# Optimization experiments

Hardware: AMD Instinct MI355X
Metric: run time of the kernel (lower is better)

Reference implementation:

```python
import jax, jax.numpy as jnp
import numpy as np

B, N, E, H = 4, 4096, 1024, 16
D = E // H            # head_dim = 64
P_DIM = 64            # proj_dim; feature dim = 2*P_DIM = 128
EPS = 1e-4


def setup_inputs() -> dict:
    key = jax.random.key(0)
    ks = jax.random.split(key, 9)
    x = jax.random.normal(ks[0], (B, N, E), jnp.float32)
    init = 0.02
    Wq = jax.random.normal(ks[1], (E, E), jnp.float32) * init
    Wk = jax.random.normal(ks[2], (E, E), jnp.float32) * init
    Wv = jax.random.normal(ks[3], (E, E), jnp.float32) * init
    Wo = jax.random.normal(ks[4], (E, E), jnp.float32) * init
    bq = jnp.zeros((E,), jnp.float32)
    bk = jnp.zeros((E,), jnp.float32)
    bv = jnp.zeros((E,), jnp.float32)
    bo = jnp.zeros((E,), jnp.float32)
    # orthogonal random projection matrix (proj_dim, head_dim), fixed (non-trainable)
    g = np.random.default_rng(0).normal(size=(P_DIM, D))
    P = jnp.asarray(np.linalg.qr(g)[0], jnp.float32)
    return dict(x=x, Wq=Wq, bq=bq, Wk=Wk, bk=bk, Wv=Wv, bv=bv, Wo=Wo, bo=bo, P=P)


def _heads(z):
    # (B, N, E) -> (B, H, N, D)
    return z.reshape(B, N, H, D).transpose(0, 2, 1, 3)


def _normalize(z):
    return z / (jnp.linalg.norm(z, axis=-1, keepdims=True) + EPS)


def reference(x, Wq, bq, Wk, bk, Wv, bv, Wo, bo, P):
    q = _heads(x @ Wq.T + bq)
    k = _heads(x @ Wk.T + bk)
    v = _heads(x @ Wv.T + bv)
    q = _normalize(q)
    k = _normalize(k)
    scale = H ** 0.25
    qp = jnp.einsum('bhnd,ed->bhne', q, P) * scale
    kp = jnp.einsum('bhnd,ed->bhne', k, P) * scale
    fscale = P_DIM ** (-0.5)   # x.shape[-1]**-0.5 with last dim = proj_dim
    qf = jnp.concatenate([jnp.sin(qp), jnp.cos(qp)], axis=-1) * fscale  # (B,H,N,2p)
    kf = jnp.concatenate([jnp.sin(kp), jnp.cos(kp)], axis=-1) * fscale
    # non-causal linear attention: q @ (k^T v)
    kv = jnp.einsum('bhme,bhmd->bhed', kf, v)          # (B,H,2p,D)
    o = jnp.einsum('bhne,bhed->bhnd', qf, kv)          # (B,H,N,D)
    o = o.transpose(0, 2, 1, 3).reshape(B, N, E)
    return o @ Wo.T + bo
```

## Files before the change

kernel.cpp:

```cpp
#include <hip/hip_runtime.h>
#include <hip/hip_bf16.h>
#include <stdint.h>


typedef __bf16 bf16x8 __attribute__((ext_vector_type(8)));
typedef float f32x4 __attribute__((ext_vector_type(4)));

#define AS1 __attribute__((address_space(1)))
#define AS3 __attribute__((address_space(3)))

__device__ __forceinline__ void gl2lds16(const void* g, void* l) {
    __builtin_amdgcn_global_load_lds((const AS1 void*)g, (AS3 void*)l, 16, 0, 0);
}

#define CFENCE asm volatile("" ::: "memory")

static constexpr int GM = 16384, GN = 1024, GK = 1024;
static constexpr int KV_SLABS = 8;

__global__ void detect_kernel(const unsigned short* __restrict__ x,
                              int* __restrict__ flag) {
    __shared__ int s;
    const int lane = threadIdx.x;
    if (lane == 0) s = 0;
    __syncthreads();
    int cnt = 0;
#pragma unroll
    for (int i = 0; i < 2; ++i) {
        const unsigned short u = x[i * 64 + lane];
        const int e = (u >> 7) & 0xFF;
        cnt += (e >= 117 && e <= 131) ? 1 : 0;
    }
    atomicAdd(&s, cnt);
    __syncthreads();
    if (lane == 0) *flag = (s >= 100) ? 1 : 0;
}

__device__ __forceinline__ void cvt8(const float* s, __hip_bfloat16* d) {
    const float4 a = *(const float4*)s;
    const float4 b = *(const float4*)(s + 4);
    union { uint4 u; __hip_bfloat16 h[8]; } pk;
    pk.h[0] = __float2bfloat16(a.x); pk.h[1] = __float2bfloat16(a.y);
    pk.h[2] = __float2bfloat16(a.z); pk.h[3] = __float2bfloat16(a.w);
    pk.h[4] = __float2bfloat16(b.x); pk.h[5] = __float2bfloat16(b.y);
    pk.h[6] = __float2bfloat16(b.z); pk.h[7] = __float2bfloat16(b.w);
    *(uint4*)d = pk.u;
}

__global__ __launch_bounds__(256) void cvt_kernel(
    const void* __restrict__ src, __hip_bfloat16* __restrict__ dst,
    int n, const int* __restrict__ flag) {
    if (*flag) return;
    const int i = (blockIdx.x * 256 + threadIdx.x) * 8;
    if (i >= n) return;
    cvt8((const float*)src + i, dst + i);
}

__global__ __launch_bounds__(256) void cvt4_kernel(
    const void* __restrict__ s0, __hip_bfloat16* __restrict__ d0,
    const void* __restrict__ s1, __hip_bfloat16* __restrict__ d1,
    const void* __restrict__ s2, __hip_bfloat16* __restrict__ d2,
    const void* __restrict__ s3, __hip_bfloat16* __restrict__ d3,
    const int* __restrict__ flag) {
    if (*flag) return;
    const int which = blockIdx.x >> 9;
    const int i = ((blockIdx.x & 511) * 256 + threadIdx.x) * 8;
    const float* s = (const float*)(which == 0 ? s0 : which == 1 ? s1
                                   : which == 2 ? s2 : s3) + i;
    __hip_bfloat16* d = (which == 0 ? d0 : which == 1 ? d1
                         : which == 2 ? d2 : d3) + i;
    cvt8(s, d);
}

__global__ __launch_bounds__(256, 2) void gemm2_kernel(
    const void* __restrict__ Adirect,
    const __hip_bfloat16* __restrict__ Acvt,
    const void* __restrict__ W0r, const __hip_bfloat16* __restrict__ W0c,
    const void* __restrict__ W1r, const __hip_bfloat16* __restrict__ W1c,
    const void* __restrict__ b0r, const void* __restrict__ b1r,
    void* __restrict__ o0, void* __restrict__ o1,
    const int* __restrict__ flag)
{
    __shared__ unsigned short smem[3 * 128 * 64];
    unsigned short* sA  = smem;
    unsigned short* sB0 = smem + 128 * 64;
    unsigned short* sB1 = smem + 2 * 128 * 64;

    const int tid  = threadIdx.x;
    const int lane = tid & 63;
    const int w    = tid >> 6;
    const int wm   = w >> 1, wn = w & 1;
    const int lr   = lane & 15, lk = lane >> 4;

    const int id    = blockIdx.x;
    const int xcd   = id & 7;
    const int slot  = id >> 3;
    const int m0    = (xcd * 16 + (slot & 15)) * 128;
    const int n0    = (slot >> 4) * 128;
    const int fl    = *flag;

    const __hip_bfloat16* A  = fl ? (const __hip_bfloat16*)Adirect : Acvt;
    const __hip_bfloat16* W0 = fl ? (const __hip_bfloat16*)W0r : W0c;
    const __hip_bfloat16* W1 = fl ? (const __hip_bfloat16*)W1r : W1c;

    f32x4 acc[2][4][4];
#pragma unroll
    for (int t = 0; t < 2; ++t)
#pragma unroll
        for (int i = 0; i < 4; ++i)
#pragma unroll
            for (int j = 0; j < 4; ++j)
                acc[t][i][j] = (f32x4){0.f, 0.f, 0.f, 0.f};

    const __hip_bfloat16* Ab  = A + (size_t)m0 * GK;
    const __hip_bfloat16* W0b = W0 + (size_t)n0 * GK;
    const __hip_bfloat16* W1b = W1 + (size_t)n0 * GK;

    for (int k0 = 0; k0 < GK; k0 += 64) {
#pragma unroll
        for (int j = 0; j < 4; ++j) {
            const int chunk = j * 256 + tid;
            const int row   = chunk >> 3;
            const int c     = chunk & 7;
            const int cs    = c ^ (row & 7);
            const size_t go = (size_t)row * GK + k0 + cs * 8;
            const int lo = (j * 256 + w * 64) * 16;
            gl2lds16(Ab  + go, (char*)sA  + lo);
            gl2lds16(W0b + go, (char*)sB0 + lo);
            gl2lds16(W1b + go, (char*)sB1 + lo);
        }
        __syncthreads();
#pragma unroll
        for (int kk = 0; kk < 64; kk += 32) {
            const int jj = ((kk >> 3) + lk) ^ (lr & 7);
            bf16x8 af[4], b0f[4], b1f[4];
#pragma unroll
            for (int i = 0; i < 4; ++i)
                af[i] = *(const bf16x8*)&sA[(wm * 64 + i * 16 + lr) * 64 + jj * 8];
#pragma unroll
            for (int j = 0; j < 4; ++j)
                b0f[j] = *(const bf16x8*)&sB0[(wn * 64 + j * 16 + lr) * 64 + jj * 8];
#pragma unroll
            for (int j = 0; j < 4; ++j)
                b1f[j] = *(const bf16x8*)&sB1[(wn * 64 + j * 16 + lr) * 64 + jj * 8];
#pragma unroll
            for (int i = 0; i < 4; ++i)
#pragma unroll
                for (int j = 0; j < 4; ++j) {
                    acc[0][i][j] = __builtin_amdgcn_mfma_f32_16x16x32_bf16(
                        af[i], b0f[j], acc[0][i][j], 0, 0, 0);
                    acc[1][i][j] = __builtin_amdgcn_mfma_f32_16x16x32_bf16(
                        af[i], b1f[j], acc[1][i][j], 0, 0, 0);
                }
        }
        __syncthreads();
    }

    __hip_bfloat16* sC = (__hip_bfloat16*)smem;
#pragma unroll
    for (int t = 0; t < 2; ++t) {
        const void* bias_raw = t ? b1r : b0r;
        void* Cout = t ? o1 : o0;
#pragma unroll
        for (int j = 0; j < 4; ++j) {
            const int col = wn * 64 + j * 16 + lr;
            const float bv = fl ? __bfloat162float(((const __hip_bfloat16*)bias_raw)[n0 + col])
                                : ((const float*)bias_raw)[n0 + col];
            const int c2 = col >> 3, o = col & 7;
#pragma unroll
            for (int i = 0; i < 4; ++i) {
                const int rb = wm * 64 + i * 16 + lk * 4;
#pragma unroll
                for (int r = 0; r < 4; ++r) {
                    const int row = rb + r;
                    sC[row * 128 + (c2 ^ (row & 7)) * 8 + o] =
                        __float2bfloat16(acc[t][i][j][r] + bv);
                }
            }
        }
        __syncthreads();
        {
            const int row = tid >> 1, hf = tid & 1;
            __hip_bfloat16* dst = (__hip_bfloat16*)Cout + (size_t)(m0 + row) * GN + n0 + hf * 64;
#pragma unroll
            for (int q = 0; q < 8; ++q) {
                const int cc = (hf * 8 + q) ^ (row & 7);
                *(uint4*)(dst + q * 8) = *(const uint4*)&sC[row * 128 + cc * 8];
            }
        }
        __syncthreads();
    }
}

__global__ __launch_bounds__(512, 2) void gemm256_kernel(
    const void* __restrict__ Adirect,
    const __hip_bfloat16* __restrict__ Acvt,
    const void* __restrict__ Wr, const __hip_bfloat16* __restrict__ Wc,
    const void* __restrict__ bias_raw,
    void* __restrict__ Cout,
    const int* __restrict__ flag, int last)
{
    __shared__ unsigned short smem[65536];

    const int tid  = threadIdx.x;
    const int lane = tid & 63;
    const int w    = tid >> 6;
    const int wm   = w >> 2, wn = w & 3;
    const int lr   = lane & 15, lk = lane >> 4;

    const int id  = blockIdx.x;
    const int xcd = id & 7;
    const int s   = id >> 3;
    const int m0  = (xcd * 8 + (s >> 2)) * 256;
    const int n0  = (s & 3) * 256;
    const int fl  = *flag;

    const __hip_bfloat16* A = fl ? (const __hip_bfloat16*)Adirect : Acvt;
    const __hip_bfloat16* W = fl ? (const __hip_bfloat16*)Wr : Wc;
    const __hip_bfloat16* Ab = A + (size_t)m0 * GK;
    const __hip_bfloat16* Wb = W + (size_t)n0 * GK;

    f32x4 acc[8][4];
#pragma unroll
    for (int i = 0; i < 8; ++i)
#pragma unroll
        for (int j = 0; j < 4; ++j)
            acc[i][j] = (f32x4){0.f, 0.f, 0.f, 0.f};

    const int jj8 = (lk ^ ((lr >> 1) & 3)) * 8;
    int offA[8], offB[4];
#pragma unroll
    for (int i = 0; i < 8; ++i)
        offA[i] = (wm * 128 + i * 16 + lr) * 32 + jj8;
#pragma unroll
    for (int j = 0; j < 4; ++j)
        offB[j] = 8192 + (wn * 64 + j * 16 + lr) * 32 + jj8;

    size_t gofs[2];
    int    ldso[2];
#pragma unroll
    for (int p = 0; p < 2; ++p) {
        const int chunk = p * 512 + tid;
        const int row   = chunk >> 2, c = chunk & 3;
        const int cs    = c ^ ((row >> 1) & 3);
        gofs[p] = (size_t)row * GK + cs * 8;
        ldso[p] = (p * 512 + w * 64) * 16;
    }

    auto stage2 = [&](int t, int part) {
        char* base = (char*)smem + (t & 3) * 32768 + ldso[part];
        const size_t go = gofs[part] + (size_t)(t * 32);
        gl2lds16(Ab + go, base);
        gl2lds16(Wb + go, base + 16384);
    };

    stage2(0, 0); stage2(0, 1);
    stage2(1, 0); stage2(1, 1);
    stage2(2, 0); stage2(2, 1);
    asm volatile("s_waitcnt vmcnt(8)" ::: "memory");
    __builtin_amdgcn_s_barrier();

    auto tile = [&](int slot, int t, bool do_stage, int gate) {
        const unsigned short* sl = smem + slot * 16384;
        bf16x8 af[4], bfr[4], af2[4];
#pragma unroll
        for (int i = 0; i < 4; ++i) af[i] = *(const bf16x8*)&sl[offA[i]];
#pragma unroll
        for (int j = 0; j < 4; ++j) bfr[j] = *(const bf16x8*)&sl[offB[j]];
        if (do_stage) stage2(t + 3, 0);
        CFENCE;
        __builtin_amdgcn_s_barrier();
        __builtin_amdgcn_s_setprio(1);
#pragma unroll
        for (int i = 0; i < 4; ++i)
#pragma unroll
            for (int j = 0; j < 4; ++j)
                acc[i][j] = __builtin_amdgcn_mfma_f32_16x16x32_bf16(
                    af[i], bfr[j], acc[i][j], 0, 0, 0);
        __builtin_amdgcn_s_setprio(0);
        CFENCE;
        __builtin_amdgcn_s_barrier();
#pragma unroll
        for (int i = 0; i < 4; ++i) af2[i] = *(const bf16x8*)&sl[offA[4 + i]];
        if (do_stage) stage2(t + 3, 1);
        if (gate == 8)      asm volatile("s_waitcnt vmcnt(8)" ::: "memory");
        else if (gate == 4) asm volatile("s_waitcnt vmcnt(4)" ::: "memory");
        else                asm volatile("s_waitcnt vmcnt(0)" ::: "memory");
        __builtin_amdgcn_s_barrier();
        __builtin_amdgcn_s_setprio(1);
#pragma unroll
        for (int i = 0; i < 4; ++i)
#pragma unroll
            for (int j = 0; j < 4; ++j)
                acc[4 + i][j] = __builtin_amdgcn_mfma_f32_16x16x32_bf16(
                    af2[i], bfr[j], acc[4 + i][j], 0, 0, 0);
        __builtin_amdgcn_s_setprio(0);
        CFENCE;
        __builtin_amdgcn_s_barrier();
    };

#pragma unroll 1
    for (int t = 0; t < 28; t += 4) {
        tile(0, t + 0, true, 8);
        tile(1, t + 1, true, 8);
        tile(2, t + 2, true, 8);
        tile(3, t + 3, true, 8);
    }
    tile(0, 28, true, 8);
    tile(1, 29, false, 4);
    tile(2, 30, false, 0);
    tile(3, 31, false, 0);

    const bool f32out = (last != 0) && (fl == 0);
    if (f32out) {
#pragma unroll
        for (int j = 0; j < 4; ++j) {
            const int col = n0 + wn * 64 + j * 16 + lr;
            const float bv = ((const float*)bias_raw)[col];
#pragma unroll
            for (int i = 0; i < 8; ++i) {
                const int rbase = m0 + wm * 128 + i * 16 + lk * 4;
#pragma unroll
                for (int r = 0; r < 4; ++r)
                    ((float*)Cout)[(size_t)(rbase + r) * GN + col] =
                        acc[i][j][r] + bv;
            }
        }
        return;
    }

    unsigned short* sC = smem;
#pragma unroll
    for (int j = 0; j < 4; ++j) {
        const int col = wn * 64 + j * 16 + lr;
        const float bv = fl ? __bfloat162float(((const __hip_bfloat16*)bias_raw)[n0 + col])
                            : ((const float*)bias_raw)[n0 + col];
        const int c_hi = col >> 3, off = col & 7;
#pragma unroll
        for (int i = 0; i < 8; ++i) {
            const int rb = wm * 128 + i * 16 + lk * 4;
#pragma unroll
            for (int r = 0; r < 4; ++r) {
                const int row = rb + r;
                const int phys = c_hi ^ (row & 7);
                __hip_bfloat16 hv = __float2bfloat16(acc[i][j][r] + bv);
                sC[row * 256 + phys * 8 + off] = *(unsigned short*)&hv;
            }
        }
    }
    __syncthreads();
    {
        const int row = tid >> 1, half = tid & 1;
        __hip_bfloat16* dst = (__hip_bfloat16*)Cout +
            (size_t)(m0 + row) * GN + n0 + half * 128;
#pragma unroll
        for (int q = 0; q < 16; ++q) {
            const int chunk = half * 16 + q;
            const int phys  = chunk ^ (row & 7);
            *(uint4*)(dst + q * 8) = *(const uint4*)&sC[row * 256 + phys * 8];
        }
    }
}

__device__ __forceinline__ void load_P(const void* Praw, int f,
                                       __hip_bfloat16* sP, int tid) {
    const int e = tid >> 2, q = tid & 3;
    union { uint4 u[2]; __hip_bfloat16 h[16]; } pk;
    if (f) {
        pk.u[0] = *(const uint4*)((const __hip_bfloat16*)Praw + e * 64 + q * 16);
        pk.u[1] = *(const uint4*)((const __hip_bfloat16*)Praw + e * 64 + q * 16 + 8);
    } else {
        const float* ps = (const float*)Praw + e * 64 + q * 16;
#pragma unroll
        for (int j = 0; j < 16; ++j) pk.h[j] = __float2bfloat16(ps[j]);
    }
    *(uint4*)&sP[e * 72 + q * 16]     = pk.u[0];
    *(uint4*)&sP[e * 72 + q * 16 + 8] = pk.u[1];
}

__device__ __forceinline__ float sumsq16(uint4 a, uint4 b) {
    union { uint4 u; __hip_bfloat16 h[8]; } x0, x1;
    x0.u = a; x1.u = b;
    float ss = 0.f;
#pragma unroll
    for (int j = 0; j < 8; ++j) {
        float v0 = __bfloat162float(x0.h[j]); ss += v0 * v0;
        float v1 = __bfloat162float(x1.h[j]); ss += v1 * v1;
    }
    return ss;
}

__global__ __launch_bounds__(256) void kv_kernel(
    const __hip_bfloat16* __restrict__ Km,
    const __hip_bfloat16* __restrict__ Vm,
    const void* __restrict__ Praw,
    float* __restrict__ PKV,
    const int* __restrict__ flag)
{
    __shared__ __hip_bfloat16 sK[64 * 72];
    __shared__ __hip_bfloat16 sVT[64 * 72];
    __shared__ __hip_bfloat16 sP[64 * 72];
    __shared__ __hip_bfloat16 sKFT[128 * 72];
    __shared__ float sRN[64];

    const int tid  = threadIdx.x;
    const int lane = tid & 63;
    const int w    = tid >> 6;
    const int lr   = lane & 15, lk = lane >> 4;
    const int bh   = blockIdx.y;
    const int b    = bh >> 4, h = bh & 15;
    const int nst  = blockIdx.x * 512;
    const int f    = *flag;
    const int n    = tid >> 2, q2 = tid & 3;

    load_P(Praw, f, sP, tid);

    f32x4 acck[2][4];
#pragma unroll
    for (int i = 0; i < 2; ++i)
#pragma unroll
        for (int j = 0; j < 4; ++j)
            acck[i][j] = (f32x4){0.f, 0.f, 0.f, 0.f};

    size_t base = ((size_t)(b * 4096 + nst + n)) * 1024 + h * 64 + q2 * 16;
    uint4 ka = *(const uint4*)(Km + base), kb = *(const uint4*)(Km + base + 8);
    uint4 va = *(const uint4*)(Vm + base), vb = *(const uint4*)(Vm + base + 8);

    for (int s = 0; s < 8; ++s) {
        __syncthreads();
        *(uint4*)&sK[n * 72 + q2 * 16]     = ka;
        *(uint4*)&sK[n * 72 + q2 * 16 + 8] = kb;
        {
            union { uint4 u[2]; __hip_bfloat16 h[16]; } vv;
            vv.u[0] = va; vv.u[1] = vb;
#pragma unroll
            for (int j = 0; j < 16; ++j) sVT[(q2 * 16 + j) * 72 + n] = vv.h[j];
        }
        {
            float ss = sumsq16(ka, kb);
            ss += __shfl_xor(ss, 1, 64);
            ss += __shfl_xor(ss, 2, 64);
            if (q2 == 0) sRN[n] = 2.0f / (sqrtf(ss) + 1e-4f);
        }
        if (s < 7) {
            base = ((size_t)(b * 4096 + nst + (s + 1) * 64 + n)) * 1024 + h * 64 + q2 * 16;
            ka = *(const uint4*)(Km + base); kb = *(const uint4*)(Km + base + 8);
            va = *(const uint4*)(Vm + base); vb = *(const uint4*)(Vm + base + 8);
        }
        {
            bf16x8 afr0 = *(const bf16x8*)&sK[(w * 16 + lr) * 72 + lk * 8];
            bf16x8 afr1 = *(const bf16x8*)&sK[(w * 16 + lr) * 72 + 32 + lk * 8];
            float rn[4];
#pragma unroll
            for (int r = 0; r < 4; ++r) rn[r] = sRN[w * 16 + lk * 4 + r];
#pragma unroll
            for (int eb = 0; eb < 4; ++eb) {
                f32x4 pa = (f32x4){0.f, 0.f, 0.f, 0.f};
                bf16x8 b0 = *(const bf16x8*)&sP[(eb * 16 + lr) * 72 + lk * 8];
                bf16x8 b1 = *(const bf16x8*)&sP[(eb * 16 + lr) * 72 + 32 + lk * 8];
                pa = __builtin_amdgcn_mfma_f32_16x16x32_bf16(afr0, b0, pa, 0, 0, 0);
                pa = __builtin_amdgcn_mfma_f32_16x16x32_bf16(afr1, b1, pa, 0, 0, 0);
                const int col = eb * 16 + lr;
#pragma unroll
                for (int r = 0; r < 4; ++r) {
                    const int row = w * 16 + lk * 4 + r;
                    float sv, cv;
                    __sincosf(pa[r] * rn[r], &sv, &cv);
                    sKFT[col * 72 + row]        = __float2bfloat16(sv * 0.125f);
                    sKFT[(col + 64) * 72 + row] = __float2bfloat16(cv * 0.125f);
                }
            }
        }
        __syncthreads();
#pragma unroll
        for (int ks = 0; ks < 2; ++ks) {
            bf16x8 a2[2], b2[4];
            a2[0] = *(const bf16x8*)&sKFT[(w * 16 + lr) * 72 + ks * 32 + lk * 8];
            a2[1] = *(const bf16x8*)&sKFT[((w + 4) * 16 + lr) * 72 + ks * 32 + lk * 8];
#pragma unroll
            for (int db = 0; db < 4; ++db)
                b2[db] = *(const bf16x8*)&sVT[(db * 16 + lr) * 72 + ks * 32 + lk * 8];
#pragma unroll
            for (int i = 0; i < 2; ++i)
#pragma unroll
                for (int db = 0; db < 4; ++db)
                    acck[i][db] = __builtin_amdgcn_mfma_f32_16x16x32_bf16(
                        a2[i], b2[db], acck[i][db], 0, 0, 0);
        }
    }

    float* out = PKV + ((size_t)blockIdx.x * 64 + bh) * 8192;
#pragma unroll
    for (int i = 0; i < 2; ++i)
#pragma unroll
        for (int db = 0; db < 4; ++db)
#pragma unroll
            for (int r = 0; r < 4; ++r) {
                const int e = (w + 4 * i) * 16 + lk * 4 + r;
                const int d = db * 16 + lr;
                out[e * 64 + d] = acck[i][db][r];
            }
}

__global__ __launch_bounds__(256) void kv_reduce_kernel(
    const float* __restrict__ PKV, float* __restrict__ gKV)
{
    const int i = (blockIdx.x * 256 + threadIdx.x) * 4;
    f32x4 s = (f32x4){0.f, 0.f, 0.f, 0.f};
#pragma unroll
    for (int sl = 0; sl < KV_SLABS; ++sl) {
        const float4 v = *(const float4*)(PKV + (size_t)sl * 64 * 8192 + i);
        s[0] += v.x; s[1] += v.y; s[2] += v.z; s[3] += v.w;
    }
    *(float4*)(gKV + i) = *(float4*)&s;
}

__global__ __launch_bounds__(256) void o_kernel(
    const __hip_bfloat16* __restrict__ Qm,
    const void* __restrict__ Praw,
    const float* __restrict__ gKV,
    __hip_bfloat16* __restrict__ O,
    const int* __restrict__ flag)
{
    __shared__ __hip_bfloat16 sQ[64 * 72];
    __shared__ __hip_bfloat16 sP[64 * 72];
    __shared__ __hip_bfloat16 sQF[64 * 136];
    __shared__ __hip_bfloat16 sKVT[64 * 136];
    __shared__ float sRN[64];

    const int tid  = threadIdx.x;
    const int lane = tid & 63;
    const int w    = tid >> 6;
    const int lr   = lane & 15, lk = lane >> 4;
    const int bh   = blockIdx.y;
    const int b    = bh >> 4, h = bh & 15;
    const int nst  = blockIdx.x * 256;
    const int f    = *flag;
    const int n    = tid >> 2, q2 = tid & 3;

    load_P(Praw, f, sP, tid);
    {
        const float* kvsrc = gKV + (size_t)bh * 8192;
        for (int t = tid; t < 8192; t += 256) {
            const int e = t >> 6, d = t & 63;
            sKVT[d * 136 + e] = __float2bfloat16(kvsrc[t]);
        }
    }

    size_t base = ((size_t)(b * 4096 + nst + n)) * 1024 + h * 64 + q2 * 16;
    uint4 qa = *(const uint4*)(Qm + base), qb = *(const uint4*)(Qm + base + 8);

    __syncthreads();

    for (int s = 0; s < 4; ++s) {
        const int gn0 = nst + s * 64;
        *(uint4*)&sQ[n * 72 + q2 * 16]     = qa;
        *(uint4*)&sQ[n * 72 + q2 * 16 + 8] = qb;
        {
            float ss = sumsq16(qa, qb);
            ss += __shfl_xor(ss, 1, 64);
            ss += __shfl_xor(ss, 2, 64);
            if (q2 == 0) sRN[n] = 2.0f / (sqrtf(ss) + 1e-4f);
        }
        if (s < 3) {
            base = ((size_t)(b * 4096 + nst + (s + 1) * 64 + n)) * 1024 + h * 64 + q2 * 16;
            qa = *(const uint4*)(Qm + base); qb = *(const uint4*)(Qm + base + 8);
        }
        {
            bf16x8 afr0 = *(const bf16x8*)&sQ[(w * 16 + lr) * 72 + lk * 8];
            bf16x8 afr1 = *(const bf16x8*)&sQ[(w * 16 + lr) * 72 + 32 + lk * 8];
            float rn[4];
#pragma unroll
            for (int r = 0; r < 4; ++r) rn[r] = sRN[w * 16 + lk * 4 + r];
#pragma unroll
            for (int eb = 0; eb < 4; ++eb) {
                f32x4 pa = (f32x4){0.f, 0.f, 0.f, 0.f};
                bf16x8 b0 = *(const bf16x8*)&sP[(eb * 16 + lr) * 72 + lk * 8];
                bf16x8 b1 = *(const bf16x8*)&sP[(eb * 16 + lr) * 72 + 32 + lk * 8];
                pa = __builtin_amdgcn_mfma_f32_16x16x32_bf16(afr0, b0, pa, 0, 0, 0);
                pa = __builtin_amdgcn_mfma_f32_16x16x32_bf16(afr1, b1, pa, 0, 0, 0);
                const int col = eb * 16 + lr;
#pragma unroll
                for (int r = 0; r < 4; ++r) {
                    const int row = w * 16 + lk * 4 + r;
                    float sv, cv;
                    __sincosf(pa[r] * rn[r], &sv, &cv);
                    sQF[row * 136 + col]      = __float2bfloat16(sv * 0.125f);
                    sQF[row * 136 + 64 + col] = __float2bfloat16(cv * 0.125f);
                }
            }
        }
        f32x4 oacc[4];
#pragma unroll
        for (int nb = 0; nb < 4; ++nb) oacc[nb] = (f32x4){0.f, 0.f, 0.f, 0.f};
#pragma unroll
        for (int ks = 0; ks < 4; ++ks) {
            bf16x8 aa = *(const bf16x8*)&sQF[(w * 16 + lr) * 136 + ks * 32 + lk * 8];
#pragma unroll
            for (int nb = 0; nb < 4; ++nb) {
                bf16x8 bb = *(const bf16x8*)&sKVT[(nb * 16 + lr) * 136 + ks * 32 + lk * 8];
                oacc[nb] = __builtin_amdgcn_mfma_f32_16x16x32_bf16(aa, bb, oacc[nb], 0, 0, 0);
            }
        }
#pragma unroll
        for (int nb = 0; nb < 4; ++nb)
#pragma unroll
            for (int r = 0; r < 4; ++r)
                sQ[(w * 16 + lk * 4 + r) * 72 + nb * 16 + lr] =
                    __float2bfloat16(oacc[nb][r]);
        {
            uint4 o0 = *(uint4*)&sQ[n * 72 + q2 * 16];
            uint4 o1 = *(uint4*)&sQ[n * 72 + q2 * 16 + 8];
            const size_t obase = ((size_t)(b * 4096 + gn0 + n)) * 1024 + h * 64 + q2 * 16;
            *(uint4*)(O + obase)     = o0;
            *(uint4*)(O + obase + 8) = o1;
        }
    }
}

extern "C" void kernel_launch(void* const* d_in, const int* in_sizes, int n_in,
                              void* d_out, int out_size, void* d_ws, size_t ws_size,
                              hipStream_t stream)
{
    (void)in_sizes; (void)n_in; (void)out_size; (void)ws_size;
    const void* x  = d_in[0];
    const void* Wq = d_in[1];
    const void* bq = d_in[2];
    const void* Wk = d_in[3];
    const void* bk = d_in[4];
    const void* Wv = d_in[5];
    const void* bv = d_in[6];
    const void* Wo = d_in[7];
    const void* bo = d_in[8];
    const void* P  = d_in[9];

    constexpr size_t XE = (size_t)GM * GN;
    constexpr size_t WE = (size_t)GN * GK;
    constexpr size_t KVE = (size_t)64 * 128 * 64;

    __hip_bfloat16* xb  = (__hip_bfloat16*)d_ws;
    __hip_bfloat16* wqb = xb + XE;
    __hip_bfloat16* wkb = wqb + WE;
    __hip_bfloat16* wvb = wkb + WE;
    __hip_bfloat16* wob = wvb + WE;
    __hip_bfloat16* R1  = wob + WE;
    __hip_bfloat16* R2  = R1 + XE;
    float* gKV = (float*)(R2 + XE);
    float* PKV = gKV + KVE;
    int* flag  = (int*)(PKV + (size_t)KV_SLABS * 64 * 8192);

    dim3 blk(256);
    hipLaunchKernelGGL(detect_kernel, dim3(1), dim3(64), 0, stream,
                       (const unsigned short*)x, flag);

    hipLaunchKernelGGL(cvt_kernel, dim3(8192), blk, 0, stream, x, xb, (int)XE, flag);
    hipLaunchKernelGGL(cvt4_kernel, dim3(2048), blk, 0, stream,
                       Wq, wqb, Wk, wkb, Wv, wvb, Wo, wob, flag);

    hipLaunchKernelGGL(gemm2_kernel, dim3(1024), blk, 0, stream,
                       x, xb, Wk, wkb, Wv, wvb, bk, bv, R1, R2, flag);
    hipLaunchKernelGGL(kv_kernel, dim3(KV_SLABS, 64), blk, 0, stream, R1, R2, P, PKV, flag);
    hipLaunchKernelGGL(kv_reduce_kernel, dim3(512), blk, 0, stream, PKV, gKV);
    hipLaunchKernelGGL(gemm256_kernel, dim3(256), dim3(512), 0, stream,
                       x, xb, Wq, wqb, bq, R2, flag, 0);
    hipLaunchKernelGGL(o_kernel, dim3(16, 64), blk, 0, stream, R2, P, gKV, R1, flag);
    hipLaunchKernelGGL(gemm256_kernel, dim3(256), dim3(512), 0, stream,
                       R1, R1, Wo, wob, bo, d_out, flag, 1);
}
```

Baseline: 364.4 us.

## Shrink single-GEMM tile to 128x256 with double buffering and split KV wider

Replaces the 256x256 four-stage GEMM used for the Q and output projections with a 128x256 tile, a two-slot LDS double buffer and a simpler per-k-step loop. This doubles the grid to 512 blocks so the GPU's compute units are better filled. It also halves per-block LDS use. The KV accumulation kernel now uses 16 slabs of 256 rows instead of 8 of 512, for more parallelism. The cost is less reuse of B tiles per block, shallower prefetch, and more partial KV slabs to reduce.

```diff
diff --git a/kernel.cpp b/kernel.cpp
--- a/kernel.cpp
+++ b/kernel.cpp
@@ -16,7 +16,7 @@
 #define CFENCE asm volatile("" ::: "memory")
 
 static constexpr int GM = 16384, GN = 1024, GK = 1024;
-static constexpr int KV_SLABS = 8;
+static constexpr int KV_SLABS = 16;
 
 __global__ void detect_kernel(const unsigned short* __restrict__ x,
                               int* __restrict__ flag) {
@@ -192,7 +192,7 @@
     }
 }
 
-__global__ __launch_bounds__(512, 2) void gemm256_kernel(
+__global__ __launch_bounds__(512, 2) void gemm1_kernel(
     const void* __restrict__ Adirect,
     const __hip_bfloat16* __restrict__ Acvt,
     const void* __restrict__ Wr, const __hip_bfloat16* __restrict__ Wc,
@@ -200,7 +200,7 @@
     void* __restrict__ Cout,
     const int* __restrict__ flag, int last)
 {
-    __shared__ unsigned short smem[65536];
+    __shared__ unsigned short smem[32768];
 
     const int tid  = threadIdx.x;
     const int lane = tid & 63;
@@ -211,8 +211,8 @@
     const int id  = blockIdx.x;
     const int xcd = id & 7;
     const int s   = id >> 3;
-    const int m0  = (xcd * 8 + (s >> 2)) * 256;
-    const int n0  = (s & 3) * 256;
+    const int m0  = (xcd * 16 + (s & 15)) * 128;
+    const int n0  = (s >> 4) * 256;
     const int fl  = *flag;
 
     const __hip_bfloat16* A = fl ? (const __hip_bfloat16*)Adirect : Acvt;
@@ -220,56 +220,47 @@
     const __hip_bfloat16* Ab = A + (size_t)m0 * GK;
     const __hip_bfloat16* Wb = W + (size_t)n0 * GK;
 
-    f32x4 acc[8][4];
-#pragma unroll
-    for (int i = 0; i < 8; ++i)
+    f32x4 acc[4][4];
+#pragma unroll
+    for (int i = 0; i < 4; ++i)
 #pragma unroll
         for (int j = 0; j < 4; ++j)
             acc[i][j] = (f32x4){0.f, 0.f, 0.f, 0.f};
 
     const int jj8 = (lk ^ ((lr >> 1) & 3)) * 8;
-    int offA[8], offB[4];
-#pragma unroll
-    for (int i = 0; i < 8; ++i)
-        offA[i] = (wm * 128 + i * 16 + lr) * 32 + jj8;
+    int offA[4], offB[4];
+#pragma unroll
+    for (int i = 0; i < 4; ++i)
+        offA[i] = (wm * 64 + i * 16 + lr) * 32 + jj8;
 #pragma unroll
     for (int j = 0; j < 4; ++j)
-        offB[j] = 8192 + (wn * 64 + j * 16 + lr) * 32 + jj8;
-
-    size_t gofs[2];
-    int    ldso[2];
+        offB[j] = 4096 + (wn * 64 + j * 16 + lr) * 32 + jj8;
+
+    const int rowA = tid >> 2, cA = tid & 3;
+    const size_t goA = (size_t)rowA * GK + (size_t)((cA ^ ((rowA >> 1) & 3)) * 8);
+    size_t goB[2];
 #pragma unroll
     for (int p = 0; p < 2; ++p) {
         const int chunk = p * 512 + tid;
         const int row   = chunk >> 2, c = chunk & 3;
-        const int cs    = c ^ ((row >> 1) & 3);
-        gofs[p] = (size_t)row * GK + cs * 8;
-        ldso[p] = (p * 512 + w * 64) * 16;
-    }
-
-    auto stage2 = [&](int t, int part) {
-        char* base = (char*)smem + (t & 3) * 32768 + ldso[part];
-        const size_t go = gofs[part] + (size_t)(t * 32);
-        gl2lds16(Ab + go, base);
-        gl2lds16(Wb + go, base + 16384);
+        goB[p] = (size_t)row * GK + (size_t)((c ^ ((row >> 1) & 3)) * 8);
+    }
+
+    auto stage = [&](int t, int slot) {
+        char* base = (char*)smem + slot * 24576;
+        const size_t k = (size_t)(t * 32);
+        gl2lds16(Ab + goA + k,    base + w * 1024);
+        gl2lds16(Wb + goB[0] + k, base + 8192 + w * 1024);
+        gl2lds16(Wb + goB[1] + k, base + 16384 + w * 1024);
     };
 
-    stage2(0, 0); stage2(0, 1);
-    stage2(1, 0); stage2(1, 1);
-    stage2(2, 0); stage2(2, 1);
-    asm volatile("s_waitcnt vmcnt(8)" ::: "memory");
-    __builtin_amdgcn_s_barrier();
-
-    auto tile = [&](int slot, int t, bool do_stage, int gate) {
-        const unsigned short* sl = smem + slot * 16384;
-        bf16x8 af[4], bfr[4], af2[4];
+    auto compute = [&](int slot) {
+        const unsigned short* sl = smem + slot * 12288;
+        bf16x8 af[4], bfr[4];
 #pragma unroll
         for (int i = 0; i < 4; ++i) af[i] = *(const bf16x8*)&sl[offA[i]];
 #pragma unroll
         for (int j = 0; j < 4; ++j) bfr[j] = *(const bf16x8*)&sl[offB[j]];
-        if (do_stage) stage2(t + 3, 0);
-        CFENCE;
-        __builtin_amdgcn_s_barrier();
         __builtin_amdgcn_s_setprio(1);
 #pragma unroll
         for (int i = 0; i < 4; ++i)
@@ -278,38 +269,28 @@
                 acc[i][j] = __builtin_amdgcn_mfma_f32_16x16x32_bf16(
                     af[i], bfr[j], acc[i][j], 0, 0, 0);
         __builtin_amdgcn_s_setprio(0);
+    };
+
+    stage(0, 0); stage(1, 1);
+    asm volatile("s_waitcnt vmcnt(3)" ::: "memory");
+    __builtin_amdgcn_s_barrier();
+
+    constexpr int NT = GK / 32;
+#pragma unroll 1
+    for (int t = 0; t < NT - 1; ++t) {
+        compute(t & 1);
         CFENCE;
         __builtin_amdgcn_s_barrier();
-#pragma unroll
-        for (int i = 0; i < 4; ++i) af2[i] = *(const bf16x8*)&sl[offA[4 + i]];
-        if (do_stage) stage2(t + 3, 1);
-        if (gate == 8)      asm volatile("s_waitcnt vmcnt(8)" ::: "memory");
-        else if (gate == 4) asm volatile("s_waitcnt vmcnt(4)" ::: "memory");
-        else                asm volatile("s_waitcnt vmcnt(0)" ::: "memory");
+        if (t < NT - 2) {
+            stage(t + 2, t & 1);
+            asm volatile("s_waitcnt vmcnt(3)" ::: "memory");
+        } else {
+            asm volatile("s_waitcnt vmcnt(0)" ::: "memory");
+        }
         __builtin_amdgcn_s_barrier();
-        __builtin_amdgcn_s_setprio(1);
-#pragma unroll
-        for (int i = 0; i < 4; ++i)
-#pragma unroll
-            for (int j = 0; j < 4; ++j)
-                acc[4 + i][j] = __builtin_amdgcn_mfma_f32_16x16x32_bf16(
-                    af2[i], bfr[j], acc[4 + i][j], 0, 0, 0);
-        __builtin_amdgcn_s_setprio(0);
-        CFENCE;
-        __builtin_amdgcn_s_barrier();
-    };
-
-#pragma unroll 1
-    for (int t = 0; t < 28; t += 4) {
-        tile(0, t + 0, true, 8);
-        tile(1, t + 1, true, 8);
-        tile(2, t + 2, true, 8);
-        tile(3, t + 3, true, 8);
-    }
-    tile(0, 28, true, 8);
-    tile(1, 29, false, 4);
-    tile(2, 30, false, 0);
-    tile(3, 31, false, 0);
+    }
+    compute((NT - 1) & 1);
+    __syncthreads();
 
     const bool f32out = (last != 0) && (fl == 0);
     if (f32out) {
@@ -318,8 +299,8 @@
             const int col = n0 + wn * 64 + j * 16 + lr;
             const float bv = ((const float*)bias_raw)[col];
 #pragma unroll
-            for (int i = 0; i < 8; ++i) {
-                const int rbase = m0 + wm * 128 + i * 16 + lk * 4;
+            for (int i = 0; i < 4; ++i) {
+                const int rbase = m0 + wm * 64 + i * 16 + lk * 4;
 #pragma unroll
                 for (int r = 0; r < 4; ++r)
                     ((float*)Cout)[(size_t)(rbase + r) * GN + col] =
@@ -337,8 +318,8 @@
                             : ((const float*)bias_raw)[n0 + col];
         const int c_hi = col >> 3, off = col & 7;
 #pragma unroll
-        for (int i = 0; i < 8; ++i) {
-            const int rb = wm * 128 + i * 16 + lk * 4;
+        for (int i = 0; i < 4; ++i) {
+            const int rb = wm * 64 + i * 16 + lk * 4;
 #pragma unroll
             for (int r = 0; r < 4; ++r) {
                 const int row = rb + r;
@@ -350,14 +331,14 @@
     }
     __syncthreads();
     {
-        const int row = tid >> 1, half = tid & 1;
+        const int row = tid >> 2, q = tid & 3;
         __hip_bfloat16* dst = (__hip_bfloat16*)Cout +
-            (size_t)(m0 + row) * GN + n0 + half * 128;
-#pragma unroll
-        for (int q = 0; q < 16; ++q) {
-            const int chunk = half * 16 + q;
+            (size_t)(m0 + row) * GN + n0 + q * 64;
+#pragma unroll
+        for (int qq = 0; qq < 8; ++qq) {
+            const int chunk = q * 8 + qq;
             const int phys  = chunk ^ (row & 7);
-            *(uint4*)(dst + q * 8) = *(const uint4*)&sC[row * 256 + phys * 8];
+            *(uint4*)(dst + qq * 8) = *(const uint4*)&sC[row * 256 + phys * 8];
         }
     }
 }
@@ -409,7 +390,7 @@
     const int lr   = lane & 15, lk = lane >> 4;
     const int bh   = blockIdx.y;
     const int b    = bh >> 4, h = bh & 15;
-    const int nst  = blockIdx.x * 512;
+    const int nst  = blockIdx.x * 256;
     const int f    = *flag;
     const int n    = tid >> 2, q2 = tid & 3;
 
@@ -426,7 +407,7 @@
     uint4 ka = *(const uint4*)(Km + base), kb = *(const uint4*)(Km + base + 8);
     uint4 va = *(const uint4*)(Vm + base), vb = *(const uint4*)(Vm + base + 8);
 
-    for (int s = 0; s < 8; ++s) {
+    for (int s = 0; s < 4; ++s) {
         __syncthreads();
         *(uint4*)&sK[n * 72 + q2 * 16]     = ka;
         *(uint4*)&sK[n * 72 + q2 * 16 + 8] = kb;
@@ -442,7 +423,7 @@
             ss += __shfl_xor(ss, 2, 64);
             if (q2 == 0) sRN[n] = 2.0f / (sqrtf(ss) + 1e-4f);
         }
-        if (s < 7) {
+        if (s < 3) {
             base = ((size_t)(b * 4096 + nst + (s + 1) * 64 + n)) * 1024 + h * 64 + q2 * 16;
             ka = *(const uint4*)(Km + base); kb = *(const uint4*)(Km + base + 8);
             va = *(const uint4*)(Vm + base); vb = *(const uint4*)(Vm + base + 8);
@@ -661,9 +642,9 @@
                        x, xb, Wk, wkb, Wv, wvb, bk, bv, R1, R2, flag);
     hipLaunchKernelGGL(kv_kernel, dim3(KV_SLABS, 64), blk, 0, stream, R1, R2, P, PKV, flag);
     hipLaunchKernelGGL(kv_reduce_kernel, dim3(512), blk, 0, stream, PKV, gKV);
-    hipLaunchKernelGGL(gemm256_kernel, dim3(256), dim3(512), 0, stream,
+    hipLaunchKernelGGL(gemm1_kernel, dim3(512), dim3(512), 0, stream,
                        x, xb, Wq, wqb, bq, R2, flag, 0);
     hipLaunchKernelGGL(o_kernel, dim3(16, 64), blk, 0, stream, R2, P, gKV, R1, flag);
-    hipLaunchKernelGGL(gemm256_kernel, dim3(256), dim3(512), 0, stream,
+    hipLaunchKernelGGL(gemm1_kernel, dim3(512), dim3(512), 0, stream,
                        R1, R1, Wo, wob, bo, d_out, flag, 1);
 }
```

After: 391.9 us. 7.5% more time.

## Double-buffer K=32 LDS stages in fused QK GEMM with prefetch overlap

Applied to the files above, without the earlier changes.

Restructures the dual-output GEMM main loop from single-buffered K=64 tiles with two barriers per iteration to double-buffered K=32 stages. The next stage's global-to-LDS loads are issued before computing the current one, with one barrier per step, so memory latency can overlap MFMA work. It also precomputes load and fragment offsets with a new XOR swizzle, and raises wave priority around the MFMA block. LDS use stays the same, but there are twice as many loop iterations and barriers, and each barrier still waits on vmcnt(0), which limits how much overlap is possible.

```diff
diff --git a/kernel.cpp b/kernel.cpp
--- a/kernel.cpp
+++ b/kernel.cpp
@@ -81,10 +81,7 @@
     void* __restrict__ o0, void* __restrict__ o1,
     const int* __restrict__ flag)
 {
-    __shared__ unsigned short smem[3 * 128 * 64];
-    unsigned short* sA  = smem;
-    unsigned short* sB0 = smem + 128 * 64;
-    unsigned short* sB1 = smem + 2 * 128 * 64;
+    __shared__ unsigned short smem[24576];
 
     const int tid  = threadIdx.x;
     const int lane = tid & 63;
@@ -116,45 +113,72 @@
     const __hip_bfloat16* W0b = W0 + (size_t)n0 * GK;
     const __hip_bfloat16* W1b = W1 + (size_t)n0 * GK;
 
-    for (int k0 = 0; k0 < GK; k0 += 64) {
-#pragma unroll
-        for (int j = 0; j < 4; ++j) {
-            const int chunk = j * 256 + tid;
-            const int row   = chunk >> 3;
-            const int c     = chunk & 7;
-            const int cs    = c ^ (row & 7);
-            const size_t go = (size_t)row * GK + k0 + cs * 8;
-            const int lo = (j * 256 + w * 64) * 16;
-            gl2lds16(Ab  + go, (char*)sA  + lo);
-            gl2lds16(W0b + go, (char*)sB0 + lo);
-            gl2lds16(W1b + go, (char*)sB1 + lo);
-        }
-        __syncthreads();
-#pragma unroll
-        for (int kk = 0; kk < 64; kk += 32) {
-            const int jj = ((kk >> 3) + lk) ^ (lr & 7);
-            bf16x8 af[4], b0f[4], b1f[4];
-#pragma unroll
-            for (int i = 0; i < 4; ++i)
-                af[i] = *(const bf16x8*)&sA[(wm * 64 + i * 16 + lr) * 64 + jj * 8];
-#pragma unroll
-            for (int j = 0; j < 4; ++j)
-                b0f[j] = *(const bf16x8*)&sB0[(wn * 64 + j * 16 + lr) * 64 + jj * 8];
-#pragma unroll
-            for (int j = 0; j < 4; ++j)
-                b1f[j] = *(const bf16x8*)&sB1[(wn * 64 + j * 16 + lr) * 64 + jj * 8];
-#pragma unroll
-            for (int i = 0; i < 4; ++i)
-#pragma unroll
-                for (int j = 0; j < 4; ++j) {
-                    acc[0][i][j] = __builtin_amdgcn_mfma_f32_16x16x32_bf16(
-                        af[i], b0f[j], acc[0][i][j], 0, 0, 0);
-                    acc[1][i][j] = __builtin_amdgcn_mfma_f32_16x16x32_bf16(
-                        af[i], b1f[j], acc[1][i][j], 0, 0, 0);
-                }
-        }
-        __syncthreads();
-    }
+    size_t goS[2];
+    int    loS[2];
+#pragma unroll
+    for (int p = 0; p < 2; ++p) {
+        const int chunk = p * 256 + tid;
+        const int row   = chunk >> 2, c = chunk & 3;
+        goS[p] = (size_t)row * GK + (size_t)((c ^ ((row >> 1) & 3)) * 8);
+        loS[p] = (p * 256 + w * 64) * 16;
+    }
+
+    auto stage = [&](int t, int sl) {
+        char* base = (char*)smem + sl * 24576;
+        const size_t k = (size_t)t * 32;
+#pragma unroll
+        for (int p = 0; p < 2; ++p) {
+            gl2lds16(Ab  + goS[p] + k, base + loS[p]);
+            gl2lds16(W0b + goS[p] + k, base + 8192 + loS[p]);
+            gl2lds16(W1b + goS[p] + k, base + 16384 + loS[p]);
+        }
+    };
+
+    const int jj8 = (lk ^ ((lr >> 1) & 3)) * 8;
+    int offA[4], offB0[4], offB1[4];
+#pragma unroll
+    for (int i = 0; i < 4; ++i) {
+        offA[i]  = (wm * 64 + i * 16 + lr) * 32 + jj8;
+        offB0[i] = 4096 + (wn * 64 + i * 16 + lr) * 32 + jj8;
+        offB1[i] = 8192 + (wn * 64 + i * 16 + lr) * 32 + jj8;
+    }
+
+    auto compute = [&](int sl) {
+        const unsigned short* s = smem + sl * 12288;
+        bf16x8 af[4], b0f[4], b1f[4];
+#pragma unroll
+        for (int i = 0; i < 4; ++i) {
+            af[i]  = *(const bf16x8*)&s[offA[i]];
+            b0f[i] = *(const bf16x8*)&s[offB0[i]];
+            b1f[i] = *(const bf16x8*)&s[offB1[i]];
+        }
+        __builtin_amdgcn_s_setprio(1);
+#pragma unroll
+        for (int i = 0; i < 4; ++i)
+#pragma unroll
+            for (int j = 0; j < 4; ++j) {
+                acc[0][i][j] = __builtin_amdgcn_mfma_f32_16x16x32_bf16(
+                    af[i], b0f[j], acc[0][i][j], 0, 0, 0);
+                acc[1][i][j] = __builtin_amdgcn_mfma_f32_16x16x32_bf16(
+                    af[i], b1f[j], acc[1][i][j], 0, 0, 0);
+            }
+        __builtin_amdgcn_s_setprio(0);
+    };
+
+    constexpr int NT = GK / 32;
+    stage(0, 0);
+    asm volatile("s_waitcnt vmcnt(0)" ::: "memory");
+    __builtin_amdgcn_s_barrier();
+
+#pragma unroll 1
+    for (int t = 0; t < NT; ++t) {
+        if (t + 1 < NT) stage(t + 1, (t + 1) & 1);
+        compute(t & 1);
+        CFENCE;
+        asm volatile("s_waitcnt vmcnt(0)" ::: "memory");
+        __builtin_amdgcn_s_barrier();
+    }
+    __syncthreads();
 
     __hip_bfloat16* sC = (__hip_bfloat16*)smem;
 #pragma unroll
```

Result: no change. 366.9 us (+0.7%).
